# Performance work log

Measured on AMD Instinct MI355X. Metric: run time of the kernel, lower is better.

The kernel has to match this reference:

```python
import jax, jax.numpy as jnp
import numpy as np

W_GRID, H_GRID = 5, 5
N_NODES = W_GRID * H_GRID  # 25
N_NEI = 8
N_CLS = 10
BN_EPS = 1e-5


def _neighbors(i, w, h):
    """Replicates Brain.neighbors ordering exactly; pads missing slots with -1
    (the torch code pads with p1 == zeros at the END of the list)."""
    size = w * h
    n = []
    if i - w >= 0:
        n.append(i - w)
    if i % w != 0:
        n.append(i - 1)
    if (i + 1) % w != 0:
        n.append(i + 1)
    if i + w < size:
        n.append(i + w)
    if i - w - 1 >= 0 and i % w != 0:
        n.append(i - w - 1)
    if i - w + 1 >= 0 and (i + 1) % w != 0:
        n.append(i - w + 1)
    if i + w - 1 < size and i % w != 0:
        n.append(i + w - 1)
    if i + w + 1 < size and (i + 1) % w != 0:
        n.append(i + w + 1)
    while len(n) < N_NEI:
        n.append(-1)
    return n

NEI = np.array([_neighbors(i, W_GRID, H_GRID) for i in range(N_NODES)], dtype=np.int32)  # [25, 8]
NEI_CLIP = np.maximum(NEI, 0)
NEI_MASK = (NEI >= 0)


def conv_bn_relu(x, W, b, g, be, m, v):
    # Conv2d(k=3, s=1, p=1) + eval-mode BatchNorm2d + ReLU, NCHW layout
    y = jax.lax.conv_general_dilated(
        x, W, window_strides=(1, 1), padding=[(1, 1), (1, 1)],
        dimension_numbers=("NCHW", "OIHW", "NCHW"))
    y = y + b[None, :, None, None]
    scale = g / jnp.sqrt(v + BN_EPS)
    y = (y - m[None, :, None, None]) * scale[None, :, None, None] + be[None, :, None, None]
    return jax.nn.relu(y)


def maxpool3s2p1(x):
    # MaxPool2d(kernel=3, stride=2, padding=1)
    return jax.lax.reduce_window(
        x, -jnp.inf, jax.lax.max,
        window_dimensions=(1, 1, 3, 3), window_strides=(1, 1, 2, 2),
        padding=[(0, 0), (0, 0), (1, 1), (1, 1)])


def per_node_mlp(inp, Wa, ba, Wb, bb):
    # inp: [25, B, 336]; distinct Linear(336,600)-Tanh-Linear(600,10)-Softmax per node
    h = jnp.tanh(jnp.einsum("nbi,nih->nbh", inp, Wa) + ba[:, None, :])
    logits = jnp.einsum("nbh,nhc->nbc", h, Wb) + bb[:, None, :]
    return jax.nn.softmax(logits, axis=-1)  # [25, B, 10]


def setup_inputs() -> dict:
    key = jax.random.key(0)
    ks = iter(jax.random.split(key, 64))
    B, C = 8192, 3
    d = {"x": jax.random.normal(next(ks), (B, C, 20, 20), jnp.float32)}
    chans = [(C, 64), (64, 128), (128, 256), (256, 256)]
    for li, (ci, co) in enumerate(chans, start=1):
        d[f"W{li}"] = jax.random.normal(next(ks), (co, ci, 3, 3), jnp.float32) * 0.05
        d[f"b{li}"] = jax.random.normal(next(ks), (co,), jnp.float32) * 0.05
        d[f"g{li}"] = jax.random.uniform(next(ks), (co,), jnp.float32, 0.5, 1.5)
        d[f"be{li}"] = jax.random.normal(next(ks), (co,), jnp.float32) * 0.1
        d[f"m{li}"] = jax.random.normal(next(ks), (co,), jnp.float32) * 0.1
        d[f"v{li}"] = jax.random.uniform(next(ks), (co,), jnp.float32, 0.5, 1.5)
    d["Wa"] = jax.random.normal(next(ks), (N_NODES, 336, 600), jnp.float32) * 0.05
    d["ba"] = jax.random.normal(next(ks), (N_NODES, 600), jnp.float32) * 0.05
    d["Wb"] = jax.random.normal(next(ks), (N_NODES, 600, N_CLS), jnp.float32) * 0.05
    d["bb"] = jax.random.normal(next(ks), (N_NODES, N_CLS), jnp.float32) * 0.05
    return d


def reference(x, W1, b1, g1, be1, m1, v1, W2, b2, g2, be2, m2, v2,
              W3, b3, g3, be3, m3, v3, W4, b4, g4, be4, m4, v4,
              Wa, ba, Wb, bb):
    c = conv_bn_relu(x, W1, b1, g1, be1, m1, v1)
    c = maxpool3s2p1(c)                      # [B, 64, 10, 10]
    c = conv_bn_relu(c, W2, b2, g2, be2, m2, v2)
    c = maxpool3s2p1(c)                      # [B, 128, 5, 5]
    c = conv_bn_relu(c, W3, b3, g3, be3, m3, v3)
    c = conv_bn_relu(c, W4, b4, g4, be4, m4, v4)  # [B, 256, 5, 5]
    B = x.shape[0]
    feats = c.reshape(B, 256, N_NODES).transpose(2, 0, 1)  # [25, B, 256]
    # Stage 1: neighbor slots are all zeros (p1..p8 = zeros)
    zeros80 = jnp.zeros((N_NODES, B, N_NEI * N_CLS), x.dtype)
    preds = per_node_mlp(jnp.concatenate([zeros80, feats], axis=-1), Wa, ba, Wb, bb)  # [25, B, 10]
    # Stage 2: gather up to 8 neighbor predictions (ordered), pad missing with zeros
    nb = preds[jnp.asarray(NEI_CLIP)]                          # [25, 8, B, 10]
    nb = jnp.where(jnp.asarray(NEI_MASK)[:, :, None, None], nb, 0.0)
    nb = nb.transpose(0, 2, 1, 3).reshape(N_NODES, B, N_NEI * N_CLS)  # [25, B, 80]
    second = per_node_mlp(jnp.concatenate([nb, feats], axis=-1), Wa, ba, Wb, bb)  # [25, B, 10]
    mean_predictions = second.mean(axis=0)  # [B, 10]
    return mean_predictions, second
```

## Files before the change

### kernel.cpp

```cpp
#include <hip/hip_runtime.h>

typedef unsigned short u16;
typedef unsigned int u32;

typedef __attribute__((ext_vector_type(8))) __bf16 bf16x8;
typedef __attribute__((ext_vector_type(4))) float f32x4;

__device__ __forceinline__ float bf2f(u16 u) {
    u32 t = ((u32)u) << 16;
    float f;
    __builtin_memcpy(&f, &t, 4);
    return f;
}
__device__ __forceinline__ u16 f2bf(float f) {
    u32 u;
    __builtin_memcpy(&u, &f, 4);
    u32 r = (u + 0x7fffu + ((u >> 16) & 1u)) >> 16;
    return (u16)r;
}
__device__ __forceinline__ float tanh_fast(float x) {
    float xc = fminf(fmaxf(x, -15.f), 15.f);
    float e = __expf(2.f * xc);
    return (e - 1.f) / (e + 1.f);
}

__device__ __forceinline__ void gld16(const u16* g, u16* l) {
    __builtin_amdgcn_global_load_lds(
        (const __attribute__((address_space(1))) u32*)(uintptr_t)g,
        (__attribute__((address_space(3))) u32*)(u32)(uintptr_t)l,
        16, 0, 0);
}


template <int EPI, int NT>
__global__ __launch_bounds__(256, 3) void gemm_bt(
    const u16* __restrict__ A, const u16* __restrict__ W, u16* __restrict__ O,
    const float* __restrict__ epiA, const float* __restrict__ epiB,
    int Kin, int N, int T, int Himg, int Wimg,
    int ldA, int ldW, int ldO,
    long long Az, long long Wz, long long Oz, int epiZ,
    int Bc, int bshift)
{
    constexpr int NJ = NT / 32;
    __shared__ __align__(16) u16 lsA[2][128 * 32];
    __shared__ __align__(16) u16 lsW[2][NT * 32];

    const int tid = threadIdx.x;
    const int z = blockIdx.z;
    A += (long long)z * Az;
    W += (long long)z * Wz;
    O += (long long)z * Oz;
    epiB += (long long)z * epiZ;

    const int m0 = blockIdx.x * 128;
    const int n0 = blockIdx.y * NT;
    const int s = m0 >> bshift;
    const int b0 = m0 & (Bc - 1);
    const int hh0 = s / Wimg, ww0 = s % Wimg;

    const int wave = tid >> 6;
    const int lane = tid & 63;
    const int mbase = (wave >> 1) * 64;
    const int nbase = (wave & 1) * (NT / 2);
    const int ln = lane & 15, qd = lane >> 4;

    const int srow = lane >> 2;
    const int sc = (((lane & 3) - ((srow >> 1) & 3)) & 3) * 8;
    const int csel = ((qd + (ln >> 1)) & 3) * 8;

    const int rowA = wave * 32 + srow;
    const int rowW = (NT == 128) ? (wave * 32 + srow) : (wave * 16 + srow);
    const int offA0 = rowA * ldA + sc;
    const int offA1 = offA0 + 16 * ldA;
    const int offW0 = rowW * ldW + sc;
    const int offW1 = offW0 + 16 * ldW;
    u16* const lA0 = &lsA[0][0] + wave * 1024;
    u16* const lW0 = (NT == 128) ? (&lsW[0][0] + wave * 1024) : (&lsW[0][0] + wave * 512);
    constexpr int LPAR_A = 128 * 32;
    constexpr int LPAR_W = NT * 32;

    auto tapvalid = [&](int t) -> bool {
        if (T != 9) return true;
        const int hh = hh0 + t / 3 - 1, ww = ww0 + t % 3 - 1;
        return hh >= 0 && hh < Himg && ww >= 0 && ww < Wimg;
    };
    auto tapA = [&](int t) -> const u16* {
        int sp = s;
        if (T == 9) sp = (hh0 + t / 3 - 1) * Wimg + (ww0 + t % 3 - 1);
        return A + (long long)(sp * Bc + b0) * ldA;
    };

    int t0 = 0;
    while (!tapvalid(t0)) ++t0;
    int nvalid = 0;
    for (int t = 0; t < T; ++t) nvalid += tapvalid(t) ? 1 : 0;
    const int KS = Kin >> 5;
    const int S = nvalid * KS;

    const u16* Ab = tapA(t0);
    const u16* Wb = W + ((long long)t0 * N + n0) * ldW;

    gld16(Ab + offA0, lA0);
    gld16(Ab + offA1, lA0 + 512);
    gld16(Wb + offW0, lW0);
    if (NT == 128) gld16(Wb + offW1, lW0 + 512);

    int ntap = t0, nkk = 0;

    f32x4 acc[4][NJ];
#pragma unroll
    for (int i = 0; i < 4; ++i)
#pragma unroll
        for (int j = 0; j < NJ; ++j)
            acc[i][j] = (f32x4){0.f, 0.f, 0.f, 0.f};

    for (int st = 0; st < S; ++st) {
        __syncthreads();
        if (st + 1 < S) {
            nkk += 32;
            if (nkk == Kin) {
                nkk = 0;
                do { ++ntap; } while (!tapvalid(ntap));
                Ab = tapA(ntap);
                Wb = W + ((long long)ntap * N + n0) * ldW;
            }
            const int pp = (st + 1) & 1;
            gld16(Ab + offA0 + nkk, lA0 + pp * LPAR_A);
            gld16(Ab + offA1 + nkk, lA0 + pp * LPAR_A + 512);
            gld16(Wb + offW0 + nkk, lW0 + pp * LPAR_W);
            if (NT == 128) gld16(Wb + offW1 + nkk, lW0 + pp * LPAR_W + 512);
        }
        const int cp = st & 1;
        bf16x8 af[4], bfr[NJ];
#pragma unroll
        for (int f = 0; f < 4; ++f)
            af[f] = *(const bf16x8*)&lsA[cp][(mbase + f * 16 + ln) * 32 + csel];
#pragma unroll
        for (int f = 0; f < NJ; ++f)
            bfr[f] = *(const bf16x8*)&lsW[cp][(nbase + f * 16 + ln) * 32 + csel];
#pragma unroll
        for (int i = 0; i < 4; ++i)
#pragma unroll
            for (int j = 0; j < NJ; ++j)
                acc[i][j] = __builtin_amdgcn_mfma_f32_16x16x32_bf16(
                    af[i], bfr[j], acc[i][j], 0, 0, 0);
    }

#pragma unroll
    for (int j = 0; j < NJ; ++j) {
        const int n = n0 + nbase + j * 16 + ln;
        const float sh = epiB[n];
        float sc2 = 1.f;
        if (EPI == 0) sc2 = epiA[n];
#pragma unroll
        for (int i = 0; i < 4; ++i) {
            const int mrow = mbase + i * 16 + qd * 4;
#pragma unroll
            for (int rr = 0; rr < 4; ++rr) {
                float v = acc[i][j][rr];
                if (EPI == 0) v = fmaxf(v * sc2 + sh, 0.f);
                else          v = tanh_fast(v + sh);
                O[(long long)(m0 + mrow + rr) * ldO + n] = f2bf(v);
            }
        }
    }
}

template <int STAGE>
__global__ __launch_bounds__(256) void logits_mfma(
    const u16* __restrict__ h, const u16* __restrict__ Wbp, const float* __restrict__ bbp,
    u16* __restrict__ preds, float* __restrict__ dout, int Bc, int gbase)
{
    __shared__ __align__(16) u16 lsA[2][128 * 32];
    __shared__ __align__(16) u16 lsW[2][16 * 32];

    const int tid = threadIdx.x;
    const int n = blockIdx.y;
    const int m0 = blockIdx.x * 128;
    const u16* A = h + ((long long)n * Bc + m0) * 640;
    const u16* Wn = Wbp + n * 16 * 640;

    const int wave = tid >> 6;
    const int lane = tid & 63;
    const int ln = lane & 15, qd = lane >> 4;
    const int srow = lane >> 2;
    const int sc = (((lane & 3) - ((srow >> 1) & 3)) & 3) * 8;
    const int csel = ((qd + (ln >> 1)) & 3) * 8;

    const int offA0 = (wave * 32 + srow) * 640 + sc;
    const int offA1 = offA0 + 16 * 640;
    const int offW0 = srow * 640 + sc;
    u16* const lA0 = &lsA[0][0] + wave * 1024;

    gld16(A + offA0, lA0);
    gld16(A + offA1, lA0 + 512);
    if (wave == 0) gld16(Wn + offW0, &lsW[0][0]);

    f32x4 acc[2];
    acc[0] = (f32x4){0.f, 0.f, 0.f, 0.f};
    acc[1] = (f32x4){0.f, 0.f, 0.f, 0.f};

    for (int st = 0; st < 20; ++st) {
        __syncthreads();
        if (st + 1 < 20) {
            const int kk = (st + 1) * 32;
            const int pp = (st + 1) & 1;
            gld16(A + offA0 + kk, lA0 + pp * 4096);
            gld16(A + offA1 + kk, lA0 + pp * 4096 + 512);
            if (wave == 0) gld16(Wn + offW0 + kk, &lsW[pp][0]);
        }
        const int cp = st & 1;
        const bf16x8 bfr = *(const bf16x8*)&lsW[cp][ln * 32 + csel];
        const bf16x8 a0 = *(const bf16x8*)&lsA[cp][(wave * 32 + ln) * 32 + csel];
        const bf16x8 a1 = *(const bf16x8*)&lsA[cp][(wave * 32 + 16 + ln) * 32 + csel];
        acc[0] = __builtin_amdgcn_mfma_f32_16x16x32_bf16(a0, bfr, acc[0], 0, 0, 0);
        acc[1] = __builtin_amdgcn_mfma_f32_16x16x32_bf16(a1, bfr, acc[1], 0, 0, 0);
    }

    const float bias = bbp[n * 16 + ln];
#pragma unroll
    for (int i = 0; i < 2; ++i) {
#pragma unroll
        for (int rr = 0; rr < 4; ++rr) {
            const float v = acc[i][rr] + bias;
            float mx = v;
#pragma unroll
            for (int mk = 1; mk < 16; mk <<= 1)
                mx = fmaxf(mx, __shfl_xor(mx, mk));
            const float e = __expf(v - mx);
            float ssum = e;
#pragma unroll
            for (int mk = 1; mk < 16; mk <<= 1)
                ssum += __shfl_xor(ssum, mk);
            const float p = e / ssum;
            const int row = m0 + wave * 32 + i * 16 + qd * 4 + rr;
            if (ln < 10) {
                if (STAGE == 1)
                    preds[((long long)n * Bc + row) * 10 + ln] = f2bf(p);
                else
                    dout[81920 + ((long long)n * 8192 + gbase + row) * 10 + ln] = p;
            }
        }
    }
}

__global__ __launch_bounds__(256) void transpose_x(
    const float* __restrict__ x, u16* __restrict__ xt, int Bc, int bshift)
{
    const int t = blockIdx.x * 256 + threadIdx.x;
    if (t >= 400 * Bc) return;
    const int s = t >> bshift;
    const int b = t & (Bc - 1);
    const u32 c0 = f2bf(x[((long long)b * 3 + 0) * 400 + s]);
    const u32 c1 = f2bf(x[((long long)b * 3 + 1) * 400 + s]);
    const u32 c2 = f2bf(x[((long long)b * 3 + 2) * 400 + s]);
    uint2 st;
    st.x = c0 | (c1 << 16);
    st.y = c2;
    *(uint2*)(xt + ((long long)s * Bc + b) * 4) = st;
}

__global__ __launch_bounds__(256) void im2col1(
    const u16* __restrict__ xt, u16* __restrict__ xcol, int Bc, int bshift)
{
    const int t = blockIdx.x * 256 + threadIdx.x;
    if (t >= 400 * Bc) return;
    const int s = t >> bshift;
    const int b = t & (Bc - 1);
    const int hh = s / 20, ww = s % 20;

    u32 p0, q0, p1, q1, p2, q2, p3, q3, p4, q4, p5, q5, p6, q6, p7, q7, p8, q8;
#define LOADTAP(T, P, Q)                                                      \
    {                                                                         \
        const int ih = hh + (T) / 3 - 1, iw = ww + (T) % 3 - 1;               \
        P = 0u; Q = 0u;                                                       \
        if (ih >= 0 && ih < 20 && iw >= 0 && iw < 20) {                       \
            const uint2 v = *(const uint2*)(xt +                              \
                ((long long)(ih * 20 + iw) * Bc + b) * 4);                    \
            P = v.x; Q = v.y;                                                 \
        }                                                                     \
    }
    LOADTAP(0, p0, q0) LOADTAP(1, p1, q1) LOADTAP(2, p2, q2)
    LOADTAP(3, p3, q3) LOADTAP(4, p4, q4) LOADTAP(5, p5, q5)
    LOADTAP(6, p6, q6) LOADTAP(7, p7, q7) LOADTAP(8, p8, q8)
#undef LOADTAP

    u16* o = xcol + (long long)t * 32;
    uint4 w;
    w.x = p0;                w.y = q0 | (p1 << 16);
    w.z = (p1 >> 16) | (q1 << 16);
    w.w = p2;
    *(uint4*)(o + 0) = w;
    w.x = q2 | (p3 << 16);   w.y = (p3 >> 16) | (q3 << 16);
    w.z = p4;                w.w = q4 | (p5 << 16);
    *(uint4*)(o + 8) = w;
    w.x = (p5 >> 16) | (q5 << 16);
    w.y = p6;                w.z = q6 | (p7 << 16);
    w.w = (p7 >> 16) | (q7 << 16);
    *(uint4*)(o + 16) = w;
    w.x = p8;                w.y = q8;
    w.z = 0u;                w.w = 0u;
    *(uint4*)(o + 24) = w;
}

template <int CH>
__global__ __launch_bounds__(256) void pool_k(
    const u16* __restrict__ src, u16* __restrict__ dst, int Bc, int Hi, int Ho)
{
    constexpr int G = CH / 8;
    const int t = blockIdx.x * 256 + threadIdx.x;
    const int cc = t & (G - 1);
    const int b = t / G;
    if (b >= Bc) return;
    const int so = blockIdx.y;
    const int ho = so / Ho, wo = so % Ho;
    float best[8];
#pragma unroll
    for (int e = 0; e < 8; ++e) best[e] = 0.f;
    for (int ph = 0; ph < 3; ++ph) {
        const int hh = 2 * ho - 1 + ph;
        if (hh < 0 || hh >= Hi) continue;
        for (int pw = 0; pw < 3; ++pw) {
            const int ww = 2 * wo - 1 + pw;
            if (ww < 0 || ww >= Hi) continue;
            const uint4 u = *(const uint4*)(src + ((long long)(hh * Hi + ww) * Bc + b) * CH + cc * 8);
            const u32 uw[4] = {u.x, u.y, u.z, u.w};
#pragma unroll
            for (int e = 0; e < 4; ++e) {
                best[2 * e]     = fmaxf(best[2 * e],     bf2f((u16)(uw[e] & 0xffff)));
                best[2 * e + 1] = fmaxf(best[2 * e + 1], bf2f((u16)(uw[e] >> 16)));
            }
        }
    }
    u32 pk[4];
#pragma unroll
    for (int e = 0; e < 4; ++e)
        pk[e] = (u32)f2bf(best[2 * e]) | (((u32)f2bf(best[2 * e + 1])) << 16);
    uint4 st;
    st.x = pk[0]; st.y = pk[1]; st.z = pk[2]; st.w = pk[3];
    *(uint4*)(dst + ((long long)so * Bc + b) * CH + cc * 8) = st;
}

__device__ __forceinline__ void neighbors5x5(int i, int* nb) {
    const int w = 5, size = 25;
    int cnt = 0;
    if (i - w >= 0) nb[cnt++] = i - w;
    if (i % w != 0) nb[cnt++] = i - 1;
    if ((i + 1) % w != 0) nb[cnt++] = i + 1;
    if (i + w < size) nb[cnt++] = i + w;
    if (i - w - 1 >= 0 && i % w != 0) nb[cnt++] = i - w - 1;
    if (i - w + 1 >= 0 && (i + 1) % w != 0) nb[cnt++] = i - w + 1;
    if (i + w - 1 < size && i % w != 0) nb[cnt++] = i + w - 1;
    if (i + w + 1 < size && (i + 1) % w != 0) nb[cnt++] = i + w + 1;
    for (; cnt < 8; ++cnt) nb[cnt] = -1;
}

__global__ __launch_bounds__(256) void gather_nb(
    const u16* __restrict__ preds, const u16* __restrict__ feats, u16* __restrict__ A2,
    int Bc, int bshift)
{
    const int g = blockIdx.x * 256 + threadIdx.x;
    if (g >= 25 * Bc) return;
    const int n = g >> bshift;
    const int b = g & (Bc - 1);
    int nb[8];
    neighbors5x5(n, nb);
    u16* dst = A2 + (long long)g * 352;
#pragma unroll
    for (int j = 0; j < 8; ++j) {
        u32* d32 = (u32*)(dst + j * 10);
        if (nb[j] >= 0) {
            const u32* s32 = (const u32*)(preds + ((long long)nb[j] * Bc + b) * 10);
#pragma unroll
            for (int q = 0; q < 5; ++q) d32[q] = s32[q];
        } else {
#pragma unroll
            for (int q = 0; q < 5; ++q) d32[q] = 0u;
        }
    }
    const uint4* fs = (const uint4*)(feats + (long long)g * 256);
    uint4* fd = (uint4*)(dst + 80);
#pragma unroll
    for (int q = 0; q < 32; ++q) fd[q] = fs[q];
    uint4 z;
    z.x = 0u; z.y = 0u; z.z = 0u; z.w = 0u;
    *(uint4*)(dst + 336) = z;
    *(uint4*)(dst + 344) = z;
}

__global__ __launch_bounds__(256) void mean_k(float* __restrict__ dout)
{
    const int t = blockIdx.x * 256 + threadIdx.x;
    float s = 0.f;
#pragma unroll
    for (int n = 0; n < 25; ++n) s += dout[81920 + n * 81920 + t];
    dout[t] = s * 0.04f;
}

__global__ void prep_bn_all(
    const float* b1, const float* g1, const float* be1, const float* m1, const float* v1,
    const float* b2, const float* g2, const float* be2, const float* m2, const float* v2,
    const float* b3, const float* g3, const float* be3, const float* m3, const float* v3,
    const float* b4, const float* g4, const float* be4, const float* m4, const float* v4,
    float* bnA, float* bnB)
{
    const int t = blockIdx.x * 256 + threadIdx.x;
    if (t >= 704) return;
    const float *bp, *gp, *bep, *mp, *vp;
    int idx;
    if (t < 64)       { bp=b1; gp=g1; bep=be1; mp=m1; vp=v1; idx=t; }
    else if (t < 192) { bp=b2; gp=g2; bep=be2; mp=m2; vp=v2; idx=t-64; }
    else if (t < 448) { bp=b3; gp=g3; bep=be3; mp=m3; vp=v3; idx=t-192; }
    else              { bp=b4; gp=g4; bep=be4; mp=m4; vp=v4; idx=t-448; }
    const float A = gp[idx] * rsqrtf(vp[idx] + 1e-5f);
    bnA[t] = A;
    bnB[t] = (bp[idx] - mp[idx]) * A + bep[idx];
}

__global__ void prep_w1col(const float* __restrict__ W1, u16* __restrict__ W1t)
{
    const int t = blockIdx.x * 256 + threadIdx.x;
    if (t >= 64 * 32) return;
    const int n = t >> 5, k = t & 31;
    u16 v = 0;
    if (k < 27) {
        const int tap = k / 3, ci = k % 3;
        v = f2bf(W1[n * 27 + ci * 9 + tap]);
    }
    W1t[t] = v;
}

__global__ void prep_convw(const float* __restrict__ W, u16* __restrict__ Wt, int Co, int Ci)
{
    const int t = blockIdx.x * 256 + threadIdx.x;
    const int tot = 9 * Co * Ci;
    if (t >= tot) return;
    const int sh = t / (Co * Ci);
    const int rem = t % (Co * Ci);
    const int co = rem / Ci, ci = rem % Ci;
    Wt[t] = f2bf(W[(long long)(co * Ci + ci) * 9 + sh]);
}

__global__ void prep_wat(const float* __restrict__ Wa, u16* __restrict__ Wat)
{
    const int t = blockIdx.x * 256 + threadIdx.x;
    if (t >= 25 * 640 * 352) return;
    const int n = t / (640 * 352);
    const int rem = t % (640 * 352);
    const int hcol = rem / 352;
    const int k = rem % 352;
    float v = 0.f;
    if (hcol < 600 && k < 336) v = Wa[((long long)n * 336 + k) * 600 + hcol];
    Wat[t] = f2bf(v);
}

__global__ void prep_ba(const float* __restrict__ ba, float* __restrict__ bap)
{
    const int t = blockIdx.x * 256 + threadIdx.x;
    if (t >= 25 * 640) return;
    const int n = t / 640, hcol = t % 640;
    bap[t] = (hcol < 600) ? ba[n * 600 + hcol] : 0.f;
}

__global__ void prep_wbt(const float* __restrict__ Wb, const float* __restrict__ bb,
                         u16* __restrict__ Wbp, float* __restrict__ bbp)
{
    const int t = blockIdx.x * 256 + threadIdx.x;
    if (t < 25 * 16 * 640) {
        const int n = t / (16 * 640);
        const int rem = t % (16 * 640);
        const int c = rem / 640, k = rem % 640;
        u16 v = 0;
        if (c < 10 && k < 600) v = f2bf(Wb[((long long)n * 600 + k) * 10 + c]);
        Wbp[t] = v;
    }
    if (t < 25 * 16) {
        const int n = t >> 4, c = t & 15;
        bbp[t] = (c < 10) ? bb[n * 10 + c] : -1e30f;
    }
}

extern "C" void kernel_launch(void* const* d_in, const int* in_sizes, int n_in,
                              void* d_out, int out_size, void* d_ws, size_t ws_size,
                              hipStream_t stream)
{
    (void)in_sizes; (void)n_in; (void)out_size;

    const float* x  = (const float*)d_in[0];
    const float* W1 = (const float*)d_in[1];
    const float* b1 = (const float*)d_in[2];
    const float* g1 = (const float*)d_in[3];
    const float* be1= (const float*)d_in[4];
    const float* m1 = (const float*)d_in[5];
    const float* v1 = (const float*)d_in[6];
    const float* W2 = (const float*)d_in[7];
    const float* b2 = (const float*)d_in[8];
    const float* g2 = (const float*)d_in[9];
    const float* be2= (const float*)d_in[10];
    const float* m2 = (const float*)d_in[11];
    const float* v2 = (const float*)d_in[12];
    const float* W3 = (const float*)d_in[13];
    const float* b3 = (const float*)d_in[14];
    const float* g3 = (const float*)d_in[15];
    const float* be3= (const float*)d_in[16];
    const float* m3 = (const float*)d_in[17];
    const float* v3 = (const float*)d_in[18];
    const float* W4 = (const float*)d_in[19];
    const float* b4 = (const float*)d_in[20];
    const float* g4 = (const float*)d_in[21];
    const float* be4= (const float*)d_in[22];
    const float* m4 = (const float*)d_in[23];
    const float* v4 = (const float*)d_in[24];
    const float* Wa = (const float*)d_in[25];
    const float* ba = (const float*)d_in[26];
    const float* Wb = (const float*)d_in[27];
    const float* bb = (const float*)d_in[28];
    float* dout = (float*)d_out;

    auto al = [](long long v) { return (v + 255LL) & ~255LL; };
    const long long fixedB = al(4096) + al(147456) + al(589824) + al(1179648) +
                             al(11264000) + al(64000) + al(2816) + al(2816) +
                             al(512000) + al(1600);
    int Bc = 256;
    for (int cand = 2048; cand >= 256; cand >>= 1) {
        long long need = fixedB + al(80000LL * cand);
        if (need <= (long long)ws_size) { Bc = cand; break; }
    }
    const int bshift = __builtin_ctz((unsigned)Bc);
    const int C = 8192 / Bc;

    char* wsp = (char*)d_ws;
    long long off = 0;
    auto alloc = [&](long long bytes) { long long o = off; off += al(bytes); return o; };
    u16* W1t  = (u16*)(wsp + alloc(4096));
    u16* Wt2  = (u16*)(wsp + alloc(147456));
    u16* Wt3  = (u16*)(wsp + alloc(589824));
    u16* Wt4  = (u16*)(wsp + alloc(1179648));
    u16* Wat  = (u16*)(wsp + alloc(11264000));
    float* bap = (float*)(wsp + alloc(64000));
    float* bnA = (float*)(wsp + alloc(2816));
    float* bnB = (float*)(wsp + alloc(2816));
    u16* Wbp  = (u16*)(wsp + alloc(512000));
    float* bbp = (float*)(wsp + alloc(1600));
    char* ch = wsp + alloc(80000LL * Bc);
    u16* xt   = (u16*)(ch + 0LL     * Bc);
    u16* xcol = (u16*)(ch + 3200LL  * Bc);
    u16* a1   = (u16*)(ch + 28800LL * Bc);
    u16* p1   = (u16*)(ch + 0LL     * Bc);
    u16* a2   = (u16*)(ch + 12800LL * Bc);
    u16* p2   = (u16*)(ch + 38400LL * Bc);
    u16* a3   = (u16*)(ch + 0LL     * Bc);
    u16* a4   = (u16*)(ch + 12800LL * Bc);
    u16* h1   = (u16*)(ch + 25600LL * Bc);
    u16* preds= (u16*)(ch + 57600LL * Bc);
    u16* A2   = (u16*)(ch + 25600LL * Bc);
    u16* h2   = (u16*)(ch + 43200LL * Bc);

    prep_bn_all<<<dim3(3), 256, 0, stream>>>(b1,g1,be1,m1,v1, b2,g2,be2,m2,v2,
                                             b3,g3,be3,m3,v3, b4,g4,be4,m4,v4, bnA, bnB);
    prep_w1col<<<dim3(8), 256, 0, stream>>>(W1, W1t);
    prep_convw<<<dim3(288),  256, 0, stream>>>(W2, Wt2, 128, 64);
    prep_convw<<<dim3(1152), 256, 0, stream>>>(W3, Wt3, 256, 128);
    prep_convw<<<dim3(2304), 256, 0, stream>>>(W4, Wt4, 256, 256);
    prep_wat<<<dim3(22000), 256, 0, stream>>>(Wa, Wat);
    prep_ba<<<dim3(63), 256, 0, stream>>>(ba, bap);
    prep_wbt<<<dim3(1000), 256, 0, stream>>>(Wb, bb, Wbp, bbp);

    for (int c = 0; c < C; ++c) {
        const float* xc = x + (long long)c * Bc * 1200;

        transpose_x<<<dim3(400 * Bc / 256), 256, 0, stream>>>(xc, xt, Bc, bshift);
        im2col1<<<dim3(400 * Bc / 256), 256, 0, stream>>>(xt, xcol, Bc, bshift);
        gemm_bt<0,64><<<dim3(400 * Bc / 128, 1), 256, 0, stream>>>(xcol, W1t, a1, bnA, bnB,
            32, 64, 1, 1, 1, 32, 32, 64, 0LL, 0LL, 0LL, 0, Bc, bshift);
        pool_k<64><<<dim3(Bc * 8 / 256, 100), 256, 0, stream>>>(a1, p1, Bc, 20, 10);

        gemm_bt<0,128><<<dim3(100 * Bc / 128, 1), 256, 0, stream>>>(p1, Wt2, a2, bnA + 64, bnB + 64,
            64, 128, 9, 10, 10, 64, 64, 128, 0LL, 0LL, 0LL, 0, Bc, bshift);
        pool_k<128><<<dim3(Bc * 16 / 256, 25), 256, 0, stream>>>(a2, p2, Bc, 10, 5);

        gemm_bt<0,128><<<dim3(25 * Bc / 128, 2), 256, 0, stream>>>(p2, Wt3, a3, bnA + 192, bnB + 192,
            128, 256, 9, 5, 5, 128, 128, 256, 0LL, 0LL, 0LL, 0, Bc, bshift);
        gemm_bt<0,128><<<dim3(25 * Bc / 128, 2), 256, 0, stream>>>(a3, Wt4, a4, bnA + 448, bnB + 448,
            256, 256, 9, 5, 5, 256, 256, 256, 0LL, 0LL, 0LL, 0, Bc, bshift);

        gemm_bt<1,128><<<dim3(Bc / 128, 5, 25), 256, 0, stream>>>(a4, Wat + 80, h1, nullptr, bap,
            256, 640, 1, 1, 1, 256, 352, 640,
            (long long)Bc * 256, 640LL * 352, (long long)Bc * 640, 640, Bc, bshift);
        logits_mfma<1><<<dim3(Bc / 128, 25), 256, 0, stream>>>(
            h1, Wbp, bbp, preds, nullptr, Bc, 0);

        gather_nb<<<dim3(25 * Bc / 256, 1), 256, 0, stream>>>(preds, a4, A2, Bc, bshift);
        gemm_bt<1,128><<<dim3(Bc / 128, 5, 25), 256, 0, stream>>>(A2, Wat, h2, nullptr, bap,
            352, 640, 1, 1, 1, 352, 352, 640,
            (long long)Bc * 352, 640LL * 352, (long long)Bc * 640, 640, Bc, bshift);
        logits_mfma<2><<<dim3(Bc / 128, 25), 256, 0, stream>>>(
            h2, Wbp, bbp, nullptr, dout, Bc, c * Bc);
    }

    mean_k<<<dim3(320), 256, 0, stream>>>(dout);
}
```

Baseline: 1.674 ms.

## Fuse first conv GEMM with BN-ReLU and 3x3 max-pool into one kernel

Adds a conv1pool kernel that, for each pooled output position, computes the conv1 GEMM at each of the 9 window positions and keeps a running max of the BN+ReLU outputs in registers. The full-resolution conv1 activation is no longer written to or read back from memory, and the separate pooling kernel launch goes away. In exchange it recomputes conv1 outputs that are shared by overlapping pool windows, about 2.25x the conv1 math, and handles padding by clamping positions, which leaves the max unchanged. Workspace offsets are reshuffled because the a1 buffer is no longer needed.

```diff
diff --git a/kernel.cpp b/kernel.cpp
--- a/kernel.cpp
+++ b/kernel.cpp
@@ -162,6 +162,107 @@
                 else          v = tanh_fast(v + sh);
                 O[(long long)(m0 + mrow + rr) * ldO + n] = f2bf(v);
             }
+        }
+    }
+}
+
+__global__ __launch_bounds__(256, 3) void conv1pool(
+    const u16* __restrict__ xcol, const u16* __restrict__ W1t, u16* __restrict__ p1,
+    const float* __restrict__ epiA, const float* __restrict__ epiB, int Bc)
+{
+    __shared__ __align__(16) u16 lsA[2][128 * 32];
+    __shared__ __align__(16) u16 lsW[64 * 32];
+
+    const int tid = threadIdx.x;
+    const int wave = tid >> 6;
+    const int lane = tid & 63;
+    const int ln = lane & 15, qd = lane >> 4;
+    const int srow = lane >> 2;
+    const int sc = (((lane & 3) - ((srow >> 1) & 3)) & 3) * 8;
+    const int csel = ((qd + (ln >> 1)) & 3) * 8;
+
+    const int b0 = blockIdx.x * 128;
+    const int so = blockIdx.y;
+    const int ho = so / 10, wo = so % 10;
+
+    auto posAt = [&](int t) -> int {
+        int hh = 2 * ho - 1 + t / 3;
+        int ww = 2 * wo - 1 + t % 3;
+        hh = hh < 0 ? 0 : (hh > 19 ? 19 : hh);
+        ww = ww < 0 ? 0 : (ww > 19 ? 19 : ww);
+        return hh * 20 + ww;
+    };
+
+    const int rowA = wave * 32 + srow;
+    const int offA0 = rowA * 32 + sc;
+    const int offA1 = offA0 + 16 * 32;
+    u16* const lA0 = &lsA[0][0] + wave * 1024;
+
+    gld16(W1t + (wave * 16 + srow) * 32 + sc, &lsW[0] + wave * 512);
+    {
+        const u16* Ab = xcol + (long long)(posAt(0) * Bc + b0) * 32;
+        gld16(Ab + offA0, lA0);
+        gld16(Ab + offA1, lA0 + 512);
+    }
+
+    const int mbase = (wave >> 1) * 64;
+    const int nbase = (wave & 1) * 32;
+
+    float sc2[2], sh[2];
+#pragma unroll
+    for (int j = 0; j < 2; ++j) {
+        const int n = nbase + j * 16 + ln;
+        sc2[j] = epiA[n];
+        sh[j] = epiB[n];
+    }
+
+    f32x4 best[4][2];
+#pragma unroll
+    for (int i = 0; i < 4; ++i)
+#pragma unroll
+        for (int j = 0; j < 2; ++j)
+            best[i][j] = (f32x4){0.f, 0.f, 0.f, 0.f};
+
+#pragma unroll
+    for (int st = 0; st < 9; ++st) {
+        __syncthreads();
+        if (st + 1 < 9) {
+            const u16* Ab = xcol + (long long)(posAt(st + 1) * Bc + b0) * 32;
+            const int pp = (st + 1) & 1;
+            gld16(Ab + offA0, lA0 + pp * (128 * 32));
+            gld16(Ab + offA1, lA0 + pp * (128 * 32) + 512);
+        }
+        const int cp = st & 1;
+        bf16x8 af[4], bfr[2];
+#pragma unroll
+        for (int f = 0; f < 4; ++f)
+            af[f] = *(const bf16x8*)&lsA[cp][(mbase + f * 16 + ln) * 32 + csel];
+#pragma unroll
+        for (int f = 0; f < 2; ++f)
+            bfr[f] = *(const bf16x8*)&lsW[(nbase + f * 16 + ln) * 32 + csel];
+#pragma unroll
+        for (int i = 0; i < 4; ++i)
+#pragma unroll
+            for (int j = 0; j < 2; ++j) {
+                f32x4 acc = (f32x4){0.f, 0.f, 0.f, 0.f};
+                acc = __builtin_amdgcn_mfma_f32_16x16x32_bf16(af[i], bfr[j], acc, 0, 0, 0);
+#pragma unroll
+                for (int rr = 0; rr < 4; ++rr) {
+                    const float v = fmaxf(acc[rr] * sc2[j] + sh[j], 0.f);
+                    best[i][j][rr] = fmaxf(best[i][j][rr], v);
+                }
+            }
+    }
+
+#pragma unroll
+    for (int j = 0; j < 2; ++j) {
+        const int n = nbase + j * 16 + ln;
+#pragma unroll
+        for (int i = 0; i < 4; ++i) {
+            const int mrow = mbase + i * 16 + qd * 4;
+#pragma unroll
+            for (int rr = 0; rr < 4; ++rr)
+                p1[(long long)(so * Bc + b0 + mrow + rr) * 64 + n] = f2bf(best[i][j][rr]);
         }
     }
 }
@@ -545,10 +646,9 @@
     char* ch = wsp + alloc(80000LL * Bc);
     u16* xt   = (u16*)(ch + 0LL     * Bc);
     u16* xcol = (u16*)(ch + 3200LL  * Bc);
-    u16* a1   = (u16*)(ch + 28800LL * Bc);
-    u16* p1   = (u16*)(ch + 0LL     * Bc);
-    u16* a2   = (u16*)(ch + 12800LL * Bc);
-    u16* p2   = (u16*)(ch + 38400LL * Bc);
+    u16* p1   = (u16*)(ch + 28800LL * Bc);
+    u16* a2   = (u16*)(ch + 0LL     * Bc);
+    u16* p2   = (u16*)(ch + 25600LL * Bc);
     u16* a3   = (u16*)(ch + 0LL     * Bc);
     u16* a4   = (u16*)(ch + 12800LL * Bc);
     u16* h1   = (u16*)(ch + 25600LL * Bc);
@@ -571,9 +671,7 @@
 
         transpose_x<<<dim3(400 * Bc / 256), 256, 0, stream>>>(xc, xt, Bc, bshift);
         im2col1<<<dim3(400 * Bc / 256), 256, 0, stream>>>(xt, xcol, Bc, bshift);
-        gemm_bt<0,64><<<dim3(400 * Bc / 128, 1), 256, 0, stream>>>(xcol, W1t, a1, bnA, bnB,
-            32, 64, 1, 1, 1, 32, 32, 64, 0LL, 0LL, 0LL, 0, Bc, bshift);
-        pool_k<64><<<dim3(Bc * 8 / 256, 100), 256, 0, stream>>>(a1, p1, Bc, 20, 10);
+        conv1pool<<<dim3(Bc / 128, 100), 256, 0, stream>>>(xcol, W1t, p1, bnA, bnB, Bc);
 
         gemm_bt<0,128><<<dim3(100 * Bc / 128, 1), 256, 0, stream>>>(p1, Wt2, a2, bnA + 64, bnB + 64,
             64, 128, 9, 10, 10, 64, 64, 128, 0LL, 0LL, 0LL, 0, Bc, bshift);
```

Result: slower. 1.895 ms (+13.2%).
